# Kernel optimization log

Measured on AMD Instinct MI355X. Metric: run time of the kernel, lower is better.

Reference implementation:

```python
import jax, jax.numpy as jnp
import numpy as np

B, S, M = 8, 2048, 256
D = 512          # input/memory feature dim
P = 512          # proj_dim
H = 8            # num_heads


def setup_inputs() -> dict:
    key = jax.random.key(0)
    ks = jax.random.split(key, 10)
    sc = 0.02
    return {
        "input_seq": jax.random.normal(ks[0], (B, S, D), jnp.float32),
        "memory_cells": jax.random.normal(ks[1], (B, M, D), jnp.float32),
        "Wk": jax.random.normal(ks[2], (D, P), jnp.float32) * sc,
        "bk": jnp.zeros((P,), jnp.float32),
        "Wv": jax.random.normal(ks[3], (D, P), jnp.float32) * sc,
        "bv": jnp.zeros((P,), jnp.float32),
        "Wq": jax.random.normal(ks[4], (H, D, P), jnp.float32) * sc,  # stacked per-head query Dense
        "bq": jnp.zeros((H, P), jnp.float32),
        "Wo": jax.random.normal(ks[5], (H * P, P), jnp.float32) * sc,
        "bo": jnp.zeros((P,), jnp.float32),
    }


def reference(input_seq, memory_cells, Wk, bk, Wv, bv, Wq, bq, Wo, bo):
    # shared key/value projections (multi-query: one K/V for all heads)
    ik = input_seq @ Wk + bk          # [B,S,P]
    mk = memory_cells @ Wk + bk       # [B,M,P]
    iv = input_seq @ Wv + bv          # [B,S,P]
    mv = memory_cells @ Wv + bv       # [B,M,P]

    # per-head queries from memory cells, all heads at once
    q = jnp.einsum('bmd,hdp->bhmp', memory_cells, Wq) + bq[None, :, None, :]  # [B,H,M,P]

    input_score = jnp.einsum('bhmp,bsp->bhms', q, ik)          # [B,H,M,S]
    self_score = jnp.sum(q * mk[:, None], axis=-1, keepdims=True)  # [B,H,M,1]
    score = jnp.concatenate([self_score, input_score], axis=-1)    # [B,H,M,S+1]
    score = score / jnp.sqrt(jnp.float32(P))
    attn = jax.nn.softmax(score, axis=-1)

    self_attn = attn[..., 0:1]                                  # [B,H,M,1]
    input_attn = attn[..., 1:]                                  # [B,H,M,S]
    val = jnp.einsum('bhms,bsp->bhmp', input_attn, iv) + self_attn * mv[:, None]

    # concat heads: [B,M,H*P]
    concat = jnp.transpose(val, (0, 2, 1, 3)).reshape(B, M, H * P)
    return concat @ Wo + bo           # [B,M,P]
```

## Files before the change

kernel.cpp:

```cpp
#include <hip/hip_runtime.h>

#define B_ 8
#define S_ 2048
#define M_ 256
#define D_ 512
#define P_ 512
#define H_ 8

#define SCALE 0.044194173824159216f

typedef __attribute__((ext_vector_type(8))) short bf16x8;
typedef __attribute__((ext_vector_type(4))) float f32x4;

static __device__ __forceinline__ float bf2f(short u) {
  union { float f; unsigned int i; } x;
  x.i = ((unsigned int)(unsigned short)u) << 16;
  return x.f;
}
static __device__ __forceinline__ short f2bf(float f) {
  union { float f; unsigned int i; } x;
  x.f = f;
  unsigned int r = (x.i + 0x7FFFu + ((x.i >> 16) & 1u)) >> 16;
  return (short)r;
}

static __device__ __forceinline__ void gll16(const short* g, short* l) {
  __builtin_amdgcn_global_load_lds(
      (const __attribute__((address_space(1))) void*)g,
      (__attribute__((address_space(3))) void*)l, 16, 0, 0);
}

#define LGKM_WAIT() asm volatile("s_waitcnt lgkmcnt(0)" ::: "memory")
#define LGKM_SYNC() do { asm volatile("s_waitcnt lgkmcnt(0)" ::: "memory"); \
                         __builtin_amdgcn_sched_barrier(0); } while (0)
#define RAW_BAR() do { asm volatile("" ::: "memory"); __builtin_amdgcn_s_barrier(); asm volatile("" ::: "memory"); } while (0)

__global__ __launch_bounds__(256) void cast_both(
    const float* __restrict__ inA, short* __restrict__ outA, int n4A,
    const float* __restrict__ inM, short* __restrict__ outM)
{
  int idx = blockIdx.x * 256 + threadIdx.x;
  const float* in = inA;
  short* out = outA;
  if (idx >= n4A) { idx -= n4A; in = inM; out = outM; }
  float4 v = ((const float4*)in)[idx];
  short o0 = f2bf(v.x), o1 = f2bf(v.y), o2 = f2bf(v.z), o3 = f2bf(v.w);
  uint2 pk;
  pk.x = (unsigned int)(unsigned short)o0 | ((unsigned int)(unsigned short)o1 << 16);
  pk.y = (unsigned int)(unsigned short)o2 | ((unsigned int)(unsigned short)o3 << 16);
  ((uint2*)out)[idx] = pk;
}

__global__ __launch_bounds__(256) void wtrans_all(
    const float* __restrict__ Wk, const float* __restrict__ Wv,
    const float* __restrict__ Wq,
    short* __restrict__ WkT, short* __restrict__ WvT, short* __restrict__ WqT)
{
  __shared__ float tile[32][33];
  const int t = threadIdx.x, tx = t & 31, ty = t >> 5;
  const int z = blockIdx.z;
  const float* inp;
  short* outp;
  if (z == 0)      { inp = Wk; outp = WkT; }
  else if (z == 1) { inp = Wv; outp = WvT; }
  else             { inp = Wq + (size_t)(z - 2) * 512 * 512;
                     outp = WqT + (size_t)(z - 2) * 512 * 512; }
  const int n0 = blockIdx.x * 32, k0 = blockIdx.y * 32;
#pragma unroll
  for (int i = 0; i < 4; ++i)
    tile[ty + 8 * i][tx] = inp[(size_t)(k0 + ty + 8 * i) * 512 + n0 + tx];
  __syncthreads();
#pragma unroll
  for (int i = 0; i < 4; ++i)
    outp[(size_t)(n0 + ty + 8 * i) * 512 + k0 + tx] = f2bf(tile[tx][ty + 8 * i]);
}

__global__ __launch_bounds__(256) void wtrans_wo(
    const float* __restrict__ in, short* __restrict__ out)
{
  __shared__ float tile[32][33];
  const int t = threadIdx.x, tx = t & 31, ty = t >> 5;
  const int n0 = blockIdx.x * 32, k0 = blockIdx.y * 32;
#pragma unroll
  for (int i = 0; i < 4; ++i)
    tile[ty + 8 * i][tx] = in[(size_t)(k0 + ty + 8 * i) * 512 + n0 + tx];
  __syncthreads();
#pragma unroll
  for (int i = 0; i < 4; ++i)
    out[(size_t)(n0 + ty + 8 * i) * 4096 + k0 + tx] = f2bf(tile[tx][ty + 8 * i]);
}

template<int MODE, int K, int N, int LDA, int LDB>
__global__ __launch_bounds__(256, 3) void gemm128(
    const short* __restrict__ Abase, const short* __restrict__ Bbase,
    const float* __restrict__ bias, void* __restrict__ Cv,
    const size_t aZ, const size_t bZ, const size_t cZ,
    float* __restrict__ Ls,
    const float* __restrict__ eselfp, const short* __restrict__ mvbp)
{
  __shared__ short As[4096];
  __shared__ short Bs[4096];
  const int t = threadIdx.x;
  const int w = t >> 6, lane = t & 63, qd = lane >> 4, ln = lane & 15;
  const int wm = (w & 1) * 64, wn = (w >> 1) * 64;

  const int n0 = blockIdx.x * 128;
  const int m0 = blockIdx.y * 128;
  const int z = blockIdx.z;
  const int bsel = z;

  const short* A  = Abase + (size_t)z * aZ;
  const short* Bp = Bbase + (size_t)bsel * bZ;

  const int rr = t >> 2, g0 = t & 3;
  const int gs0 = g0 ^ ((rr >> 1) & 3);
  const int gs1 = g0 ^ (((rr + 64) >> 1) & 3);
  const short* ga0 = A + (size_t)(m0 + rr) * LDA + gs0 * 8;
  const short* ga1 = A + (size_t)(m0 + rr + 64) * LDA + gs1 * 8;
  const short* gb0 = Bp + (size_t)(n0 + rr) * LDB + gs0 * 8;
  const short* gb1 = Bp + (size_t)(n0 + rr + 64) * LDB + gs1 * 8;

  int aoff[4], boff[4];
#pragma unroll
  for (int mt = 0; mt < 4; ++mt) {
    int r = wm + mt * 16 + ln;
    aoff[mt] = r * 32 + (qd ^ ((r >> 1) & 3)) * 8;
  }
#pragma unroll
  for (int nt = 0; nt < 4; ++nt) {
    int r = wn + nt * 16 + ln;
    boff[nt] = r * 32 + (qd ^ ((r >> 1) & 3)) * 8;
  }

  f32x4 acc[4][4];
#pragma unroll
  for (int mt = 0; mt < 4; ++mt)
#pragma unroll
    for (int nt = 0; nt < 4; ++nt) acc[mt][nt] = (f32x4){0.f, 0.f, 0.f, 0.f};

  for (int kc = 0; kc < K; kc += 32) {
    __syncthreads();
    gll16(ga0 + kc, &As[w * 512]);
    gll16(ga1 + kc, &As[2048 + w * 512]);
    gll16(gb0 + kc, &Bs[w * 512]);
    gll16(gb1 + kc, &Bs[2048 + w * 512]);
    __syncthreads();

    bf16x8 af[4], bfr[4];
#pragma unroll
    for (int mt = 0; mt < 4; ++mt) af[mt] = *(const bf16x8*)&As[aoff[mt]];
#pragma unroll
    for (int nt = 0; nt < 4; ++nt) bfr[nt] = *(const bf16x8*)&Bs[boff[nt]];
#pragma unroll
    for (int mt = 0; mt < 4; ++mt)
#pragma unroll
      for (int nt = 0; nt < 4; ++nt)
        acc[mt][nt] = __builtin_amdgcn_mfma_f32_16x16x32_bf16(af[mt], bfr[nt], acc[mt][nt], 0, 0, 0);
  }

  if constexpr (MODE == 5) {
#pragma unroll
    for (int nt = 0; nt < 4; ++nt) {
      const int col = n0 + wn + nt * 16 + ln;
#pragma unroll
      for (int mt = 0; mt < 4; ++mt)
#pragma unroll
        for (int r = 0; r < 4; ++r) {
          const int row = m0 + wm + mt * 16 + qd * 4 + r;
          ((float*)Cv)[(size_t)z * cZ + (size_t)row * N + col] = acc[mt][nt][r];
        }
    }
  } else {
#pragma unroll
    for (int nt = 0; nt < 4; ++nt) {
      const int col = n0 + wn + nt * 16 + ln;
      const float bc = bias[512 * z + col];
#pragma unroll
      for (int mt = 0; mt < 4; ++mt)
#pragma unroll
        for (int r = 0; r < 4; ++r) {
          const int row = m0 + wm + mt * 16 + qd * 4 + r;
          const int bidx = row >> 8, ml = row & 255;
          ((short*)Cv)[((size_t)(bidx * H_ + z) * M_ + ml) * N + col] = f2bf(acc[mt][nt][r] + bc);
        }
    }
  }
}

template<int MH, int NH>
static __device__ __forceinline__ void mfma_quad(
    f32x4 (&acc)[8][4], const bf16x8 (&a)[4][2], const bf16x8 (&bfr)[2][2])
{
  __builtin_amdgcn_s_setprio(1);
#pragma unroll
  for (int kk = 0; kk < 2; ++kk)
#pragma unroll
    for (int mt = 0; mt < 4; ++mt)
#pragma unroll
      for (int nt = 0; nt < 2; ++nt)
        acc[MH * 4 + mt][NH * 2 + nt] = __builtin_amdgcn_mfma_f32_16x16x32_bf16(
            a[mt][kk], bfr[nt][kk], acc[MH * 4 + mt][NH * 2 + nt], 0, 0, 0);
  __builtin_amdgcn_s_setprio(0);
}

template<int MH, int NT>
static __device__ __forceinline__ void mfma_oct(
    f32x4 (&acc)[8][2], const bf16x8 (&a)[4][2], const bf16x8 (&bv)[2])
{
  __builtin_amdgcn_s_setprio(1);
#pragma unroll
  for (int kk = 0; kk < 2; ++kk)
#pragma unroll
    for (int mt = 0; mt < 4; ++mt)
      acc[MH * 4 + mt][NT] = __builtin_amdgcn_mfma_f32_16x16x32_bf16(
          a[mt][kk], bv[kk], acc[MH * 4 + mt][NT], 0, 0, 0);
  __builtin_amdgcn_s_setprio(0);
}

template<int NKT>
__global__ __launch_bounds__(512, 2) void qk256(
    const short* __restrict__ Abase, const short* __restrict__ Bbase,
    short* __restrict__ Eb, float* __restrict__ Ls)
{
  __shared__ short lds[65536];
  const int t = threadIdx.x;
  const int w = t >> 6, lane = t & 63, qd = lane >> 4, ln = lane & 15;
  const int wr = w >> 2, wc = w & 3;
  const int b = blockIdx.x;
  const int n0 = blockIdx.y * 256, m0 = blockIdx.z * 256;

  const short* A  = Abase + (size_t)b * (2048 * 512) + (size_t)m0 * 512;
  const short* Bp = Bbase + (size_t)b * (2048 * 512) + (size_t)n0 * 512;

  const int s0 = w * 64 + lane, s1 = s0 + 512;
  const int sr0 = s0 >> 3, sc0 = ((s0 & 7) ^ (sr0 & 7)) * 8;
  const int sr1 = s1 >> 3, sc1 = ((s1 & 7) ^ (sr1 & 7)) * 8;
  auto stage = [&](const short* g, short* lbase) {
    gll16(g + (size_t)sr0 * 512 + sc0, lbase + w * 512);
    gll16(g + (size_t)sr1 * 512 + sc1, lbase + 4096 + w * 512);
  };

  const int cq0 = ((qd    ) ^ (ln & 7)) * 8;
  const int cq1 = ((4 + qd) ^ (ln & 7)) * 8;
  const int brow = (wc & 1) * 64;

  f32x4 acc[8][4];
#pragma unroll
  for (int i = 0; i < 8; ++i)
#pragma unroll
    for (int j = 0; j < 4; ++j) acc[i][j] = (f32x4){0.f, 0.f, 0.f, 0.f};

  stage(A,                  &lds[0]);
  stage(A + 128 * 512,      &lds[8192]);
  stage(Bp,                 &lds[32768]);
  stage(Bp + 128 * 512,     &lds[32768 + 8192]);
  stage(A + 64,             &lds[16384]);
  stage(A + 128 * 512 + 64, &lds[16384 + 8192]);
  asm volatile("s_waitcnt vmcnt(4)" ::: "memory");
  __builtin_amdgcn_s_barrier();

#pragma unroll 1
  for (int kt = 0; kt < NKT; ++kt) {
    const int p = kt & 1;
    short* Ah = &lds[p * 16384 + wr * 8192];
    short* Bh = &lds[32768 + p * 16384 + (wc >> 1) * 8192];
    bf16x8 a[4][2], bfr[2][2];

#pragma unroll
    for (int mt = 0; mt < 4; ++mt) {
      a[mt][0] = *(const bf16x8*)&Ah[(mt * 16 + ln) * 64 + cq0];
      a[mt][1] = *(const bf16x8*)&Ah[(mt * 16 + ln) * 64 + cq1];
    }
#pragma unroll
    for (int nt = 0; nt < 2; ++nt) {
      bfr[nt][0] = *(const bf16x8*)&Bh[(brow + nt * 16 + ln) * 64 + cq0];
      bfr[nt][1] = *(const bf16x8*)&Bh[(brow + nt * 16 + ln) * 64 + cq1];
    }
    if (kt + 1 < NKT) {
      stage(Bp + (kt + 1) * 64,             &lds[32768 + (p ^ 1) * 16384]);
      stage(Bp + 128 * 512 + (kt + 1) * 64, &lds[32768 + (p ^ 1) * 16384 + 8192]);
    }
    RAW_BAR(); LGKM_SYNC();
    mfma_quad<0, 0>(acc, a, bfr);
    RAW_BAR();

#pragma unroll
    for (int nt = 0; nt < 2; ++nt) {
      bfr[nt][0] = *(const bf16x8*)&Bh[(brow + 32 + nt * 16 + ln) * 64 + cq0];
      bfr[nt][1] = *(const bf16x8*)&Bh[(brow + 32 + nt * 16 + ln) * 64 + cq1];
    }
    RAW_BAR(); LGKM_SYNC();
    mfma_quad<0, 1>(acc, a, bfr);
    RAW_BAR();

#pragma unroll
    for (int mt = 0; mt < 4; ++mt) {
      a[mt][0] = *(const bf16x8*)&Ah[4096 + (mt * 16 + ln) * 64 + cq0];
      a[mt][1] = *(const bf16x8*)&Ah[4096 + (mt * 16 + ln) * 64 + cq1];
    }
    RAW_BAR(); LGKM_SYNC();
    mfma_quad<1, 1>(acc, a, bfr);
    RAW_BAR();

#pragma unroll
    for (int nt = 0; nt < 2; ++nt) {
      bfr[nt][0] = *(const bf16x8*)&Bh[(brow + nt * 16 + ln) * 64 + cq0];
      bfr[nt][1] = *(const bf16x8*)&Bh[(brow + nt * 16 + ln) * 64 + cq1];
    }
    if (kt + 2 < NKT) {
      stage(A + (kt + 2) * 64,             &lds[p * 16384]);
      stage(A + 128 * 512 + (kt + 2) * 64, &lds[p * 16384 + 8192]);
    }
    RAW_BAR(); LGKM_SYNC();
    mfma_quad<1, 0>(acc, a, bfr);
    if (kt + 2 < NKT) { asm volatile("s_waitcnt vmcnt(4)" ::: "memory"); }
    else              { asm volatile("s_waitcnt vmcnt(0)" ::: "memory"); }
    RAW_BAR();
  }

#pragma unroll
  for (int i = 0; i < 8; ++i)
#pragma unroll
    for (int j = 0; j < 4; ++j)
#pragma unroll
      for (int r = 0; r < 4; ++r)
        acc[i][j][r] = __expf(acc[i][j][r] * SCALE);
#pragma unroll
  for (int i = 0; i < 8; ++i)
#pragma unroll
    for (int r = 0; r < 4; ++r) {
      float rs = acc[i][0][r] + acc[i][1][r] + acc[i][2][r] + acc[i][3][r];
      rs += __shfl_xor(rs, 1);
      rs += __shfl_xor(rs, 2);
      rs += __shfl_xor(rs, 4);
      rs += __shfl_xor(rs, 8);
      if (ln == 0) {
        const int row = m0 + wr * 128 + i * 16 + qd * 4 + r;
        atomicAdd(&Ls[(size_t)b * 2048 + row], rs);
      }
    }
#pragma unroll
  for (int i = 0; i < 8; ++i)
#pragma unroll
    for (int j = 0; j < 4; ++j)
#pragma unroll
      for (int r = 0; r < 4; ++r) {
        const int row = wr * 128 + i * 16 + qd * 4 + r;
        const int col = wc * 64 + j * 16 + ln;
        lds[row * 256 + (col ^ ((row & 7) << 3))] = f2bf(acc[i][j][r]);
      }
  LGKM_WAIT();
  RAW_BAR();
  short* Cb = Eb + (size_t)b * 2048 * 2048;
#pragma unroll
  for (int it = 0; it < 16; ++it) {
    const int flat = it * 512 + t;
    const int row = flat >> 5, c = flat & 31;
    bf16x8 v = *(const bf16x8*)&lds[row * 256 + ((c ^ (row & 7)) * 8)];
    *(bf16x8*)(Cb + (size_t)(m0 + row) * 2048 + n0 + c * 8) = v;
  }
}

template<int NKT>
__global__ __launch_bounds__(512, 2) void pv128(
    const short* __restrict__ Abase, const short* __restrict__ Bbase,
    short* __restrict__ valb, const float* __restrict__ Ls,
    const float* __restrict__ eselfp, const short* __restrict__ mvbp)
{
  __shared__ short lds[49152];
  const int t = threadIdx.x;
  const int w = t >> 6, lane = t & 63, qd = lane >> 4, ln = lane & 15;
  const int wr = w >> 2, wc = w & 3;
  const int b = blockIdx.x;
  const int n0 = blockIdx.y * 128;
  const int bz = blockIdx.z;
  const int m0 = bz * 256;

  const short* A  = Abase + (size_t)b * (2048 * 2048) + (size_t)m0 * 2048;
  const short* Bp = Bbase + (size_t)b * (512 * 2048) + (size_t)n0 * 2048;

  const int s0 = w * 64 + lane, s1 = s0 + 512;
  const int sr0 = s0 >> 3, sc0 = ((s0 & 7) ^ (sr0 & 7)) * 8;
  const int sr1 = s1 >> 3, sc1 = ((s1 & 7) ^ (sr1 & 7)) * 8;
  auto stage = [&](const short* g, short* lbase) {
    gll16(g + (size_t)sr0 * 2048 + sc0, lbase + w * 512);
    gll16(g + (size_t)sr1 * 2048 + sc1, lbase + 4096 + w * 512);
  };

  const int cq0 = ((qd    ) ^ (ln & 7)) * 8;
  const int cq1 = ((4 + qd) ^ (ln & 7)) * 8;
  const int brow = wc * 32;

  f32x4 acc[8][2];
#pragma unroll
  for (int i = 0; i < 8; ++i)
#pragma unroll
    for (int j = 0; j < 2; ++j) acc[i][j] = (f32x4){0.f, 0.f, 0.f, 0.f};

  stage(A,                   &lds[0]);
  stage(A + 128 * 2048,      &lds[8192]);
  stage(Bp,                  &lds[32768]);
  stage(A + 64,              &lds[16384]);
  stage(A + 128 * 2048 + 64, &lds[16384 + 8192]);
  asm volatile("s_waitcnt vmcnt(4)" ::: "memory");
  __builtin_amdgcn_s_barrier();

#pragma unroll 1
  for (int kt = 0; kt < NKT; ++kt) {
    const int p = kt & 1;
    short* Ah = &lds[p * 16384 + wr * 8192];
    short* Bh = &lds[32768 + p * 8192];
    bf16x8 a[4][2], bv[2];

#pragma unroll
    for (int mt = 0; mt < 4; ++mt) {
      a[mt][0] = *(const bf16x8*)&Ah[(mt * 16 + ln) * 64 + cq0];
      a[mt][1] = *(const bf16x8*)&Ah[(mt * 16 + ln) * 64 + cq1];
    }
    bv[0] = *(const bf16x8*)&Bh[(brow + ln) * 64 + cq0];
    bv[1] = *(const bf16x8*)&Bh[(brow + ln) * 64 + cq1];
    if (kt + 1 < NKT)
      stage(Bp + (kt + 1) * 64, &lds[32768 + (p ^ 1) * 8192]);
    RAW_BAR(); LGKM_SYNC();
    mfma_oct<0, 0>(acc, a, bv);
    RAW_BAR();

    bv[0] = *(const bf16x8*)&Bh[(brow + 16 + ln) * 64 + cq0];
    bv[1] = *(const bf16x8*)&Bh[(brow + 16 + ln) * 64 + cq1];
    RAW_BAR(); LGKM_SYNC();
    mfma_oct<0, 1>(acc, a, bv);
    RAW_BAR();

#pragma unroll
    for (int mt = 0; mt < 4; ++mt) {
      a[mt][0] = *(const bf16x8*)&Ah[4096 + (mt * 16 + ln) * 64 + cq0];
      a[mt][1] = *(const bf16x8*)&Ah[4096 + (mt * 16 + ln) * 64 + cq1];
    }
    RAW_BAR(); LGKM_SYNC();
    mfma_oct<1, 1>(acc, a, bv);
    RAW_BAR();

    bv[0] = *(const bf16x8*)&Bh[(brow + ln) * 64 + cq0];
    bv[1] = *(const bf16x8*)&Bh[(brow + ln) * 64 + cq1];
    if (kt + 2 < NKT) {
      stage(A + (kt + 2) * 64,              &lds[p * 16384]);
      stage(A + 128 * 2048 + (kt + 2) * 64, &lds[p * 16384 + 8192]);
    }
    RAW_BAR(); LGKM_SYNC();
    mfma_oct<1, 0>(acc, a, bv);
    if (kt + 2 < NKT) { asm volatile("s_waitcnt vmcnt(4)" ::: "memory"); }
    else              { asm volatile("s_waitcnt vmcnt(0)" ::: "memory"); }
    RAW_BAR();
  }

#pragma unroll
  for (int i = 0; i < 8; ++i)
#pragma unroll
    for (int r = 0; r < 4; ++r) {
      const int row = wr * 128 + i * 16 + qd * 4 + r;
      const float es  = eselfp[(size_t)b * 2048 + m0 + row];
      const float inv = 1.f / (es + Ls[(size_t)b * 2048 + m0 + row]);
      const short* mvr = mvbp + ((size_t)(b * 256 + row)) * 512;
#pragma unroll
      for (int j = 0; j < 2; ++j) {
        const int lcol = wc * 32 + j * 16 + ln;
        const float v = (acc[i][j][r] + es * bf2f(mvr[n0 + lcol])) * inv;
        lds[row * 128 + (lcol ^ ((row & 7) << 3))] = f2bf(v);
      }
    }
  LGKM_WAIT();
  RAW_BAR();
#pragma unroll
  for (int it = 0; it < 8; ++it) {
    const int flat = it * 512 + t;
    const int row = flat >> 4, c = flat & 15;
    bf16x8 v = *(const bf16x8*)&lds[row * 128 + ((c ^ (row & 7)) * 8)];
    *(bf16x8*)(valb + ((size_t)(b * 256 + row)) * 4096 + (size_t)bz * 512 + n0 + c * 8) = v;
  }
}

template<bool TRANSV>
__global__ __launch_bounds__(256, 3) void proj_kv(
    const short* __restrict__ A,
    const short* __restrict__ WkT, const short* __restrict__ WvT,
    const float* __restrict__ bk, const float* __restrict__ bv,
    short* __restrict__ Ck, short* __restrict__ Cvv)
{
  __shared__ short Sh[8192];
  short* As  = Sh;
  short* Bks = Sh + 4096;
  short* Bvs = Sh + 6144;
  const int t = threadIdx.x;
  const int w = t >> 6, lane = t & 63, qd = lane >> 4, ln = lane & 15;
  const int n0 = blockIdx.x * 64, m0 = blockIdx.y * 128;
  const int wm = (w & 1) * 64, wn2 = (w >> 1) * 32;

  const int rr = t >> 2, g0 = t & 3;
  const int gs0 = g0 ^ ((rr >> 1) & 3);
  const int gs1 = g0 ^ (((rr + 64) >> 1) & 3);
  const short* ga0 = A + (size_t)(m0 + rr) * 512 + gs0 * 8;
  const short* ga1 = A + (size_t)(m0 + rr + 64) * 512 + gs1 * 8;
  const short* gbk = WkT + (size_t)(n0 + rr) * 512 + gs0 * 8;
  const short* gbv = WvT + (size_t)(n0 + rr) * 512 + gs0 * 8;

  int aoff[4], boff[2];
#pragma unroll
  for (int mt = 0; mt < 4; ++mt) {
    int r = wm + mt * 16 + ln;
    aoff[mt] = r * 32 + (qd ^ ((r >> 1) & 3)) * 8;
  }
#pragma unroll
  for (int nt = 0; nt < 2; ++nt) {
    int r = wn2 + nt * 16 + ln;
    boff[nt] = r * 32 + (qd ^ ((r >> 1) & 3)) * 8;
  }

  f32x4 accK[4][2], accV[4][2];
#pragma unroll
  for (int mt = 0; mt < 4; ++mt)
#pragma unroll
    for (int nt = 0; nt < 2; ++nt) {
      accK[mt][nt] = (f32x4){0.f, 0.f, 0.f, 0.f};
      accV[mt][nt] = (f32x4){0.f, 0.f, 0.f, 0.f};
    }

  for (int kc = 0; kc < 512; kc += 32) {
    __syncthreads();
    gll16(ga0 + kc, &As[w * 512]);
    gll16(ga1 + kc, &As[2048 + w * 512]);
    gll16(gbk + kc, &Bks[w * 512]);
    gll16(gbv + kc, &Bvs[w * 512]);
    __syncthreads();

    bf16x8 af[4], bkf[2], bvf[2];
#pragma unroll
    for (int mt = 0; mt < 4; ++mt) af[mt] = *(const bf16x8*)&As[aoff[mt]];
#pragma unroll
    for (int nt = 0; nt < 2; ++nt) {
      bkf[nt] = *(const bf16x8*)&Bks[boff[nt]];
      bvf[nt] = *(const bf16x8*)&Bvs[boff[nt]];
    }
#pragma unroll
    for (int mt = 0; mt < 4; ++mt)
#pragma unroll
      for (int nt = 0; nt < 2; ++nt) {
        accK[mt][nt] = __builtin_amdgcn_mfma_f32_16x16x32_bf16(af[mt], bkf[nt], accK[mt][nt], 0, 0, 0);
        accV[mt][nt] = __builtin_amdgcn_mfma_f32_16x16x32_bf16(af[mt], bvf[nt], accV[mt][nt], 0, 0, 0);
      }
  }

#pragma unroll
  for (int nt = 0; nt < 2; ++nt) {
    const int col = n0 + wn2 + nt * 16 + ln;
    const float bc = bk[col];
#pragma unroll
    for (int mt = 0; mt < 4; ++mt)
#pragma unroll
      for (int r = 0; r < 4; ++r) {
        const int row = m0 + wm + mt * 16 + qd * 4 + r;
        Ck[(size_t)row * 512 + col] = f2bf(accK[mt][nt][r] + bc);
      }
  }

  if constexpr (!TRANSV) {
#pragma unroll
    for (int nt = 0; nt < 2; ++nt) {
      const int col = n0 + wn2 + nt * 16 + ln;
      const float bc = bv[col];
#pragma unroll
      for (int mt = 0; mt < 4; ++mt)
#pragma unroll
        for (int r = 0; r < 4; ++r) {
          const int row = m0 + wm + mt * 16 + qd * 4 + r;
          Cvv[(size_t)row * 512 + col] = f2bf(accV[mt][nt][r] + bc);
        }
    }
  } else {
    __syncthreads();
    short* ep = &Sh[w * 1280];
    const int lr = lane >> 1, lc16 = (lane & 1) * 16;
#pragma unroll
    for (int pass = 0; pass < 2; ++pass) {
#pragma unroll
      for (int mh = 0; mh < 2; ++mh) {
        const int mt = pass * 2 + mh;
#pragma unroll
        for (int nt = 0; nt < 2; ++nt) {
          const float bc = bv[n0 + wn2 + nt * 16 + ln];
#pragma unroll
          for (int r = 0; r < 4; ++r)
            ep[(nt * 16 + ln) * 40 + mh * 16 + qd * 4 + r] = f2bf(accV[mt][nt][r] + bc);
        }
      }
      LGKM_WAIT();
      const int srow0 = m0 + wm + pass * 32;
      const int bidx = srow0 >> 11;
      const int sloc = (srow0 & 2047) + lc16;
      const int pcol = n0 + wn2 + lr;
      short* outp = Cvv + (size_t)bidx * P_ * S_ + (size_t)pcol * S_ + sloc;
      *(bf16x8*)outp = *(const bf16x8*)&ep[lr * 40 + lc16];
      *(bf16x8*)(outp + 8) = *(const bf16x8*)&ep[lr * 40 + lc16 + 8];
      LGKM_WAIT();
    }
  }
}

__global__ __launch_bounds__(256) void reduce_wo(
    const float* __restrict__ partial, const float* __restrict__ bo,
    float* __restrict__ out)
{
  const int idx4 = blockIdx.x * 256 + threadIdx.x;
  float4 s = ((const float4*)bo)[idx4 & 127];
#pragma unroll
  for (int zz = 0; zz < 4; ++zz) {
    float4 p = ((const float4*)partial)[(size_t)zz * 262144 + idx4];
    s.x += p.x; s.y += p.y; s.z += p.z; s.w += p.w;
  }
  ((float4*)out)[idx4] = s;
}

__global__ __launch_bounds__(256) void selfscore(
    const short* __restrict__ qb, const short* __restrict__ mkb,
    float* __restrict__ eself, float* __restrict__ Ls)
{
  const int z = blockIdx.x, t = threadIdx.x;
  const short* qr = qb + ((size_t)z * M_ + t) * P_;
  const short* mr = mkb + ((size_t)(z >> 3) * M_ + t) * P_;
  float s = 0.f;
#pragma unroll 8
  for (int c = 0; c < P_; c += 8) {
    bf16x8 qv = *(const bf16x8*)(qr + c);
    bf16x8 mv = *(const bf16x8*)(mr + c);
#pragma unroll
    for (int j = 0; j < 8; ++j) s += bf2f(qv[j]) * bf2f(mv[j]);
  }
  eself[(size_t)z * M_ + t] = __expf(s * SCALE);
  Ls[(size_t)z * M_ + t] = 0.f;
}

extern "C" void kernel_launch(void* const* d_in, const int* in_sizes, int n_in,
                              void* d_out, int out_size, void* d_ws, size_t ws_size,
                              hipStream_t stream) {
  const float* input_seq = (const float*)d_in[0];
  const float* memcells  = (const float*)d_in[1];
  const float* Wk = (const float*)d_in[2];
  const float* bk = (const float*)d_in[3];
  const float* Wv = (const float*)d_in[4];
  const float* bv = (const float*)d_in[5];
  const float* Wq = (const float*)d_in[6];
  const float* bq = (const float*)d_in[7];
  const float* Wo = (const float*)d_in[8];
  const float* bo = (const float*)d_in[9];
  float* out = (float*)d_out;

  short* ws = (short*)d_ws;
  size_t o = 0;
  short* valb = ws + o; o += (size_t)B_ * M_ * H_ * P_;
  short* WoT  = ws + o; o += (size_t)(H_ * P_) * P_;
  short* mvb  = ws + o; o += (size_t)B_ * M_ * P_;
  short* mkb  = ws + o; o += (size_t)B_ * M_ * P_;
  short* qb   = ws + o; o += (size_t)B_ * H_ * M_ * P_;
  short* ivT  = ws + o; o += (size_t)B_ * P_ * S_;
  short* ikb  = ws + o; o += (size_t)B_ * S_ * P_;
  float* partial = (float*)(ws + o); o += (size_t)B_ * H_ * M_ * P_;
  float* eself = (float*)(ws + o); o += 2 * (size_t)B_ * H_ * M_;
  float* Ls    = (float*)(ws + o); o += 2 * (size_t)B_ * H_ * M_;
  short* region2 = ws + o;
  short* Ab  = region2;
  short* Mb  = Ab + (size_t)B_ * S_ * D_;
  short* WkT = Mb + (size_t)B_ * M_ * D_;
  short* WvT = WkT + (size_t)D_ * P_;
  short* WqT = WvT + (size_t)D_ * P_;
  short* Eb  = region2;

  dim3 blk(256);

  const int n4A = B_ * S_ * D_ / 4;
  const int n4M = B_ * M_ * D_ / 4;
  cast_both<<<dim3((n4A + n4M) / 256), blk, 0, stream>>>(input_seq, Ab, n4A, memcells, Mb);
  wtrans_all<<<dim3(16, 16, 10), blk, 0, stream>>>(Wk, Wv, Wq, WkT, WvT, WqT);
  wtrans_wo<<<dim3(16, 128), blk, 0, stream>>>(Wo, WoT);

  proj_kv<true><<<dim3(8, 128), blk, 0, stream>>>(Ab, WkT, WvT, bk, bv, ikb, ivT);
  proj_kv<false><<<dim3(8, 16), blk, 0, stream>>>(Mb, WkT, WvT, bk, bv, mkb, mvb);

  gemm128<1, 512, 512, 512, 512><<<dim3(4, 16, 8), blk, 0, stream>>>(
      Mb, WqT, bq, qb, 0, (size_t)D_ * P_, 0, nullptr, nullptr, nullptr);

  selfscore<<<dim3(64), blk, 0, stream>>>(qb, mkb, eself, Ls);

  qk256<8><<<dim3(8, 8, 8), dim3(512), 0, stream>>>(qb, ikb, Eb, Ls);

  pv128<32><<<dim3(8, 4, 8), dim3(512), 0, stream>>>(Eb, ivT, valb, Ls, eself, mvb);

  gemm128<5, 1024, 512, 4096, 4096><<<dim3(4, 16, 4), blk, 0, stream>>>(
      valb, WoT, nullptr, partial, 1024, 1024,
      (size_t)2048 * 512, nullptr, nullptr, nullptr);
  reduce_wo<<<dim3(1024), blk, 0, stream>>>(partial, bo, out);
}
```

Before: 305.1 us.

## Simplify QK and PV main loops to single-barrier double-buffered k-steps

Replaces the four-phase ping-pong schedule in qk256 and the PV kernel, which had many barriers and lgkm waits per k-tile, with a simpler loop. Each iteration prefetches the next A and B tiles, loads fragments for two k-halves and issues all MFMAs, then ends with one combined vmcnt/lgkmcnt wait and a single barrier. The PV kernel also changes its wave layout from 2x4 to 4x2, so each wave owns a 64x64 output tile, which raises B-fragment reuse. The aim is to cut barrier and wait overhead, at the cost of a full vmcnt(0) stall each iteration and less explicit overlap between loads and MFMAs.

```diff
diff --git a/kernel.cpp b/kernel.cpp
--- a/kernel.cpp
+++ b/kernel.cpp
@@ -31,8 +31,7 @@
 }
 
 #define LGKM_WAIT() asm volatile("s_waitcnt lgkmcnt(0)" ::: "memory")
-#define LGKM_SYNC() do { asm volatile("s_waitcnt lgkmcnt(0)" ::: "memory"); \
-                         __builtin_amdgcn_sched_barrier(0); } while (0)
+#define VMLG_WAIT() asm volatile("s_waitcnt vmcnt(0) lgkmcnt(0)" ::: "memory")
 #define RAW_BAR() do { asm volatile("" ::: "memory"); __builtin_amdgcn_s_barrier(); asm volatile("" ::: "memory"); } while (0)
 
 __global__ __launch_bounds__(256) void cast_both(
@@ -187,36 +186,6 @@
   }
 }
 
-template<int MH, int NH>
-static __device__ __forceinline__ void mfma_quad(
-    f32x4 (&acc)[8][4], const bf16x8 (&a)[4][2], const bf16x8 (&bfr)[2][2])
-{
-  __builtin_amdgcn_s_setprio(1);
-#pragma unroll
-  for (int kk = 0; kk < 2; ++kk)
-#pragma unroll
-    for (int mt = 0; mt < 4; ++mt)
-#pragma unroll
-      for (int nt = 0; nt < 2; ++nt)
-        acc[MH * 4 + mt][NH * 2 + nt] = __builtin_amdgcn_mfma_f32_16x16x32_bf16(
-            a[mt][kk], bfr[nt][kk], acc[MH * 4 + mt][NH * 2 + nt], 0, 0, 0);
-  __builtin_amdgcn_s_setprio(0);
-}
-
-template<int MH, int NT>
-static __device__ __forceinline__ void mfma_oct(
-    f32x4 (&acc)[8][2], const bf16x8 (&a)[4][2], const bf16x8 (&bv)[2])
-{
-  __builtin_amdgcn_s_setprio(1);
-#pragma unroll
-  for (int kk = 0; kk < 2; ++kk)
-#pragma unroll
-    for (int mt = 0; mt < 4; ++mt)
-      acc[MH * 4 + mt][NT] = __builtin_amdgcn_mfma_f32_16x16x32_bf16(
-          a[mt][kk], bv[kk], acc[MH * 4 + mt][NT], 0, 0, 0);
-  __builtin_amdgcn_s_setprio(0);
-}
-
 template<int NKT>
 __global__ __launch_bounds__(512, 2) void qk256(
     const short* __restrict__ Abase, const short* __restrict__ Bbase,
@@ -250,13 +219,11 @@
 #pragma unroll
     for (int j = 0; j < 4; ++j) acc[i][j] = (f32x4){0.f, 0.f, 0.f, 0.f};
 
-  stage(A,                  &lds[0]);
-  stage(A + 128 * 512,      &lds[8192]);
-  stage(Bp,                 &lds[32768]);
-  stage(Bp + 128 * 512,     &lds[32768 + 8192]);
-  stage(A + 64,             &lds[16384]);
-  stage(A + 128 * 512 + 64, &lds[16384 + 8192]);
-  asm volatile("s_waitcnt vmcnt(4)" ::: "memory");
+  stage(A,              &lds[0]);
+  stage(A + 128 * 512,  &lds[8192]);
+  stage(Bp,             &lds[32768]);
+  stage(Bp + 128 * 512, &lds[32768 + 8192]);
+  asm volatile("s_waitcnt vmcnt(0)" ::: "memory");
   __builtin_amdgcn_s_barrier();
 
 #pragma unroll 1
@@ -264,57 +231,44 @@
     const int p = kt & 1;
     short* Ah = &lds[p * 16384 + wr * 8192];
     short* Bh = &lds[32768 + p * 16384 + (wc >> 1) * 8192];
-    bf16x8 a[4][2], bfr[2][2];
-
-#pragma unroll
-    for (int mt = 0; mt < 4; ++mt) {
-      a[mt][0] = *(const bf16x8*)&Ah[(mt * 16 + ln) * 64 + cq0];
-      a[mt][1] = *(const bf16x8*)&Ah[(mt * 16 + ln) * 64 + cq1];
-    }
-#pragma unroll
-    for (int nt = 0; nt < 2; ++nt) {
-      bfr[nt][0] = *(const bf16x8*)&Bh[(brow + nt * 16 + ln) * 64 + cq0];
-      bfr[nt][1] = *(const bf16x8*)&Bh[(brow + nt * 16 + ln) * 64 + cq1];
-    }
+
+    bf16x8 a0[8], b0[4];
+#pragma unroll
+    for (int j = 0; j < 4; ++j)
+      b0[j] = *(const bf16x8*)&Bh[(brow + j * 16 + ln) * 64 + cq0];
+#pragma unroll
+    for (int mt = 0; mt < 8; ++mt)
+      a0[mt] = *(const bf16x8*)&Ah[(mt * 16 + ln) * 64 + cq0];
     if (kt + 1 < NKT) {
-      stage(Bp + (kt + 1) * 64,             &lds[32768 + (p ^ 1) * 16384]);
-      stage(Bp + 128 * 512 + (kt + 1) * 64, &lds[32768 + (p ^ 1) * 16384 + 8192]);
-    }
-    RAW_BAR(); LGKM_SYNC();
-    mfma_quad<0, 0>(acc, a, bfr);
-    RAW_BAR();
-
-#pragma unroll
-    for (int nt = 0; nt < 2; ++nt) {
-      bfr[nt][0] = *(const bf16x8*)&Bh[(brow + 32 + nt * 16 + ln) * 64 + cq0];
-      bfr[nt][1] = *(const bf16x8*)&Bh[(brow + 32 + nt * 16 + ln) * 64 + cq1];
-    }
-    RAW_BAR(); LGKM_SYNC();
-    mfma_quad<0, 1>(acc, a, bfr);
-    RAW_BAR();
-
-#pragma unroll
-    for (int mt = 0; mt < 4; ++mt) {
-      a[mt][0] = *(const bf16x8*)&Ah[4096 + (mt * 16 + ln) * 64 + cq0];
-      a[mt][1] = *(const bf16x8*)&Ah[4096 + (mt * 16 + ln) * 64 + cq1];
-    }
-    RAW_BAR(); LGKM_SYNC();
-    mfma_quad<1, 1>(acc, a, bfr);
-    RAW_BAR();
-
-#pragma unroll
-    for (int nt = 0; nt < 2; ++nt) {
-      bfr[nt][0] = *(const bf16x8*)&Bh[(brow + nt * 16 + ln) * 64 + cq0];
-      bfr[nt][1] = *(const bf16x8*)&Bh[(brow + nt * 16 + ln) * 64 + cq1];
-    }
-    if (kt + 2 < NKT) {
-      stage(A + (kt + 2) * 64,             &lds[p * 16384]);
-      stage(A + 128 * 512 + (kt + 2) * 64, &lds[p * 16384 + 8192]);
-    }
-    RAW_BAR(); LGKM_SYNC();
-    mfma_quad<1, 0>(acc, a, bfr);
-    if (kt + 2 < NKT) { asm volatile("s_waitcnt vmcnt(4)" ::: "memory"); }
-    else              { asm volatile("s_waitcnt vmcnt(0)" ::: "memory"); }
+      stage(A  + (size_t)(kt + 1) * 64,             &lds[(p ^ 1) * 16384]);
+      stage(A  + 128 * 512 + (size_t)(kt + 1) * 64, &lds[(p ^ 1) * 16384 + 8192]);
+      stage(Bp + (size_t)(kt + 1) * 64,             &lds[32768 + (p ^ 1) * 16384]);
+      stage(Bp + 128 * 512 + (size_t)(kt + 1) * 64, &lds[32768 + (p ^ 1) * 16384 + 8192]);
+    }
+    __builtin_amdgcn_s_setprio(1);
+#pragma unroll
+    for (int mt = 0; mt < 8; ++mt)
+#pragma unroll
+      for (int j = 0; j < 4; ++j)
+        acc[mt][j] = __builtin_amdgcn_mfma_f32_16x16x32_bf16(a0[mt], b0[j], acc[mt][j], 0, 0, 0);
+    __builtin_amdgcn_s_setprio(0);
+
+    bf16x8 a1[8], b1[4];
+#pragma unroll
+    for (int j = 0; j < 4; ++j)
+      b1[j] = *(const bf16x8*)&Bh[(brow + j * 16 + ln) * 64 + cq1];
+#pragma unroll
+    for (int mt = 0; mt < 8; ++mt)
+      a1[mt] = *(const bf16x8*)&Ah[(mt * 16 + ln) * 64 + cq1];
+    __builtin_amdgcn_s_setprio(1);
+#pragma unroll
+    for (int mt = 0; mt < 8; ++mt)
+#pragma unroll
+      for (int j = 0; j < 4; ++j)
+        acc[mt][j] = __builtin_amdgcn_mfma_f32_16x16x32_bf16(a1[mt], b1[j], acc[mt][j], 0, 0, 0);
+    __builtin_amdgcn_s_setprio(0);
+
+    VMLG_WAIT();
     RAW_BAR();
   }
 
@@ -370,7 +324,7 @@
   __shared__ short lds[49152];
   const int t = threadIdx.x;
   const int w = t >> 6, lane = t & 63, qd = lane >> 4, ln = lane & 15;
-  const int wr = w >> 2, wc = w & 3;
+  const int wr = w >> 1, wc = w & 1;
   const int b = blockIdx.x;
   const int n0 = blockIdx.y * 128;
   const int bz = blockIdx.z;
@@ -389,82 +343,76 @@
 
   const int cq0 = ((qd    ) ^ (ln & 7)) * 8;
   const int cq1 = ((4 + qd) ^ (ln & 7)) * 8;
-  const int brow = wc * 32;
-
-  f32x4 acc[8][2];
-#pragma unroll
-  for (int i = 0; i < 8; ++i)
-#pragma unroll
-    for (int j = 0; j < 2; ++j) acc[i][j] = (f32x4){0.f, 0.f, 0.f, 0.f};
-
-  stage(A,                   &lds[0]);
-  stage(A + 128 * 2048,      &lds[8192]);
-  stage(Bp,                  &lds[32768]);
-  stage(A + 64,              &lds[16384]);
-  stage(A + 128 * 2048 + 64, &lds[16384 + 8192]);
-  asm volatile("s_waitcnt vmcnt(4)" ::: "memory");
+
+  f32x4 acc[4][4];
+#pragma unroll
+  for (int i = 0; i < 4; ++i)
+#pragma unroll
+    for (int j = 0; j < 4; ++j) acc[i][j] = (f32x4){0.f, 0.f, 0.f, 0.f};
+
+  stage(A,               &lds[0]);
+  stage(A + 128 * 2048,  &lds[8192]);
+  stage(Bp,              &lds[32768]);
+  asm volatile("s_waitcnt vmcnt(0)" ::: "memory");
   __builtin_amdgcn_s_barrier();
 
 #pragma unroll 1
   for (int kt = 0; kt < NKT; ++kt) {
     const int p = kt & 1;
-    short* Ah = &lds[p * 16384 + wr * 8192];
+    short* Ah = &lds[p * 16384 + (wr >> 1) * 8192 + (wr & 1) * 4096];
     short* Bh = &lds[32768 + p * 8192];
-    bf16x8 a[4][2], bv[2];
-
-#pragma unroll
-    for (int mt = 0; mt < 4; ++mt) {
-      a[mt][0] = *(const bf16x8*)&Ah[(mt * 16 + ln) * 64 + cq0];
-      a[mt][1] = *(const bf16x8*)&Ah[(mt * 16 + ln) * 64 + cq1];
-    }
-    bv[0] = *(const bf16x8*)&Bh[(brow + ln) * 64 + cq0];
-    bv[1] = *(const bf16x8*)&Bh[(brow + ln) * 64 + cq1];
-    if (kt + 1 < NKT)
-      stage(Bp + (kt + 1) * 64, &lds[32768 + (p ^ 1) * 8192]);
-    RAW_BAR(); LGKM_SYNC();
-    mfma_oct<0, 0>(acc, a, bv);
+
+    bf16x8 a0[4], b0[4];
+#pragma unroll
+    for (int j = 0; j < 4; ++j)
+      b0[j] = *(const bf16x8*)&Bh[(wc * 64 + j * 16 + ln) * 64 + cq0];
+#pragma unroll
+    for (int mt = 0; mt < 4; ++mt)
+      a0[mt] = *(const bf16x8*)&Ah[(mt * 16 + ln) * 64 + cq0];
+    if (kt + 1 < NKT) {
+      stage(A  + (size_t)(kt + 1) * 64,              &lds[(p ^ 1) * 16384]);
+      stage(A  + 128 * 2048 + (size_t)(kt + 1) * 64, &lds[(p ^ 1) * 16384 + 8192]);
+      stage(Bp + (size_t)(kt + 1) * 64,              &lds[32768 + (p ^ 1) * 8192]);
+    }
+    __builtin_amdgcn_s_setprio(1);
+#pragma unroll
+    for (int mt = 0; mt < 4; ++mt)
+#pragma unroll
+      for (int j = 0; j < 4; ++j)
+        acc[mt][j] = __builtin_amdgcn_mfma_f32_16x16x32_bf16(a0[mt], b0[j], acc[mt][j], 0, 0, 0);
+    __builtin_amdgcn_s_setprio(0);
+
+    bf16x8 a1[4], b1[4];
+#pragma unroll
+    for (int j = 0; j < 4; ++j)
+      b1[j] = *(const bf16x8*)&Bh[(wc * 64 + j * 16 + ln) * 64 + cq1];
+#pragma unroll
+    for (int mt = 0; mt < 4; ++mt)
+      a1[mt] = *(const bf16x8*)&Ah[(mt * 16 + ln) * 64 + cq1];
+    __builtin_amdgcn_s_setprio(1);
+#pragma unroll
+    for (int mt = 0; mt < 4; ++mt)
+#pragma unroll
+      for (int j = 0; j < 4; ++j)
+        acc[mt][j] = __builtin_amdgcn_mfma_f32_16x16x32_bf16(a1[mt], b1[j], acc[mt][j], 0, 0, 0);
+    __builtin_amdgcn_s_setprio(0);
+
+    VMLG_WAIT();
     RAW_BAR();
-
-    bv[0] = *(const bf16x8*)&Bh[(brow + 16 + ln) * 64 + cq0];
-    bv[1] = *(const bf16x8*)&Bh[(brow + 16 + ln) * 64 + cq1];
-    RAW_BAR(); LGKM_SYNC();
-    mfma_oct<0, 1>(acc, a, bv);
-    RAW_BAR();
-
-#pragma unroll
-    for (int mt = 0; mt < 4; ++mt) {
-      a[mt][0] = *(const bf16x8*)&Ah[4096 + (mt * 16 + ln) * 64 + cq0];
-      a[mt][1] = *(const bf16x8*)&Ah[4096 + (mt * 16 + ln) * 64 + cq1];
-    }
-    RAW_BAR(); LGKM_SYNC();
-    mfma_oct<1, 1>(acc, a, bv);
-    RAW_BAR();
-
-    bv[0] = *(const bf16x8*)&Bh[(brow + ln) * 64 + cq0];
-    bv[1] = *(const bf16x8*)&Bh[(brow + ln) * 64 + cq1];
-    if (kt + 2 < NKT) {
-      stage(A + (kt + 2) * 64,              &lds[p * 16384]);
-      stage(A + 128 * 2048 + (kt + 2) * 64, &lds[p * 16384 + 8192]);
-    }
-    RAW_BAR(); LGKM_SYNC();
-    mfma_oct<1, 0>(acc, a, bv);
-    if (kt + 2 < NKT) { asm volatile("s_waitcnt vmcnt(4)" ::: "memory"); }
-    else              { asm volatile("s_waitcnt vmcnt(0)" ::: "memory"); }
-    RAW_BAR();
-  }
-
-#pragma unroll
-  for (int i = 0; i < 8; ++i)
+  }
+
+#pragma unroll
+  for (int mt = 0; mt < 4; ++mt)
 #pragma unroll
     for (int r = 0; r < 4; ++r) {
-      const int row = wr * 128 + i * 16 + qd * 4 + r;
+      const int row = wr * 64 + mt * 16 + qd * 4 + r;
       const float es  = eselfp[(size_t)b * 2048 + m0 + row];
       const float inv = 1.f / (es + Ls[(size_t)b * 2048 + m0 + row]);
       const short* mvr = mvbp + ((size_t)(b * 256 + row)) * 512;
 #pragma unroll
-      for (int j = 0; j < 2; ++j) {
-        const int lcol = wc * 32 + j * 16 + ln;
-        const float v = (acc[i][j][r] + es * bf2f(mvr[n0 + lcol])) * inv;
+      for (int j = 0; j < 4; ++j) {
+        const int lcol = wc * 64 + j * 16 + ln;
+        const float v = (acc[mt][j][r] + es * bf2f(mvr[n0 + lcol])) * inv;
         lds[row * 128 + (lcol ^ ((row & 7) << 3))] = f2bf(v);
       }
     }
```

Result: no change. 305.8 us (+0.2%).
